# Optimization experiments

Measured on AMD Instinct MI355X. Metric: run time of the kernel, lower is better.

The kernel has to match this reference:

```python
import jax, jax.numpy as jnp
import numpy as np

N_NODES = 50000
N_EDGES = 800000
D_NODE = 128
D_EDGE = 128
D_OUT = 256
HID = 256


def setup_inputs() -> dict:
    key = jax.random.key(0)
    ks = jax.random.split(key, 10)
    s1 = 1.0 / np.sqrt(D_NODE + D_EDGE)
    s2 = 1.0 / np.sqrt(HID)
    s3 = 1.0 / np.sqrt(D_NODE + HID)
    return {
        "x": jax.random.normal(ks[0], (N_NODES, D_NODE), dtype=jnp.float32),
        "edge_index": jax.random.randint(ks[1], (2, N_EDGES), 0, N_NODES, dtype=jnp.int64),
        "edge_attr": jax.random.normal(ks[2], (N_EDGES, D_EDGE), dtype=jnp.float32),
        "u": jax.random.normal(ks[3], (1, 64), dtype=jnp.float32),
        "batch": jnp.zeros((N_NODES,), dtype=jnp.int64),
        "w1a": jax.random.normal(ks[4], (D_NODE + D_EDGE, HID), dtype=jnp.float32) * s1,
        "b1a": jnp.zeros((HID,), dtype=jnp.float32),
        "w1b": jax.random.normal(ks[5], (HID, HID), dtype=jnp.float32) * s2,
        "b1b": jnp.zeros((HID,), dtype=jnp.float32),
        "w2a": jax.random.normal(ks[6], (D_NODE + HID, HID), dtype=jnp.float32) * s3,
        "b2a": jnp.zeros((HID,), dtype=jnp.float32),
        "w2b": jax.random.normal(ks[7], (HID, D_OUT), dtype=jnp.float32) * s2,
        "b2b": jnp.zeros((D_OUT,), dtype=jnp.float32),
    }


def reference(x, edge_index, edge_attr, u, batch, w1a, b1a, w1b, b1b, w2a, b2a, w2b, b2b):
    row, col = edge_index[0], edge_index[1]
    # edge-wise MLP: [E, D_NODE + D_EDGE] -> 256 -> 256
    h = jnp.concatenate([x[row], edge_attr], axis=1)
    h = jax.nn.elu(h @ w1a + b1a) @ w1b + b1b  # [E, 256]
    # scatter_mean over destination nodes (dim_size = N)
    n = x.shape[0]
    sums = jax.ops.segment_sum(h, col, num_segments=n)  # [N, 256]
    cnt = jax.ops.segment_sum(jnp.ones((h.shape[0],), h.dtype), col, num_segments=n)
    mean = sums / jnp.maximum(cnt, 1.0)[:, None]
    # node-wise MLP: [N, D_NODE + 256] -> 256 -> D_OUT
    z = jnp.concatenate([x, mean], axis=1)
    return jax.nn.elu(z @ w2a + b2a) @ w2b + b2b
```

## Files before the change

### kernel.cpp

```cpp
#include <hip/hip_runtime.h>
#include <hip/hip_bf16.h>

#define N_NODES 50000
#define N_EDGES 800000

typedef short s16x8 __attribute__((ext_vector_type(8)));
typedef short s16x4 __attribute__((ext_vector_type(4)));
typedef float f32x4 __attribute__((ext_vector_type(4)));

__device__ __forceinline__ unsigned short f2bf(float f) {
    union { float f; unsigned u; } v; v.f = f;
    unsigned r = v.u + 0x7fffu + ((v.u >> 16) & 1u);
    return (unsigned short)(r >> 16);
}

__device__ __forceinline__ float bf2f(unsigned short u) {
    union { unsigned u; float f; } v; v.u = ((unsigned)u) << 16;
    return v.f;
}

__device__ __forceinline__ s16x8 ld8(const unsigned short* p) {
    return *(const s16x8*)p;
}

__device__ __forceinline__ float elu(float h) {
    return h > 0.0f ? h : (__expf(h) - 1.0f);
}

__global__ void wconv_kernel(const float* __restrict__ src,
                             unsigned short* __restrict__ dst,
                             int K, int N) {
    int idx = blockIdx.x * 256 + threadIdx.x;
    if (idx >= K * N) return;
    int n = idx / K;
    int k = idx - n * K;
    dst[idx] = f2bf(src[k * N + n]);
}

__global__ void hist_kernel(const int* __restrict__ ei, int* __restrict__ hist) {
    int e = blockIdx.x * 256 + threadIdx.x;
    if (e < N_EDGES) atomicAdd(&hist[ei[N_EDGES + e]], 1);
}

__global__ void scan_kernel(const int* __restrict__ hist, int* __restrict__ cursor) {
    __shared__ int tmp[1024];
    __shared__ int carryS;
    const int t = threadIdx.x;
    if (t == 0) carryS = 0;
    __syncthreads();
    for (int base = 0; base < N_NODES; base += 4096) {
        int i = base + t * 4;
        int4 v = {0, 0, 0, 0};
        if (i + 3 < N_NODES) v = *(const int4*)&hist[i];
        else {
            v.x = (i + 0 < N_NODES) ? hist[i + 0] : 0;
            v.y = (i + 1 < N_NODES) ? hist[i + 1] : 0;
            v.z = (i + 2 < N_NODES) ? hist[i + 2] : 0;
            v.w = (i + 3 < N_NODES) ? hist[i + 3] : 0;
        }
        int s = v.x + v.y + v.z + v.w;
        tmp[t] = s;
        __syncthreads();
        for (int off = 1; off < 1024; off <<= 1) {
            int add = (t >= off) ? tmp[t - off] : 0;
            __syncthreads();
            tmp[t] += add;
            __syncthreads();
        }
        int incl = tmp[t];
        int excl0 = carryS + incl - s;
        if (i     < N_NODES) cursor[i]     = excl0;
        if (i + 1 < N_NODES) cursor[i + 1] = excl0 + v.x;
        if (i + 2 < N_NODES) cursor[i + 2] = excl0 + v.x + v.y;
        if (i + 3 < N_NODES) cursor[i + 3] = excl0 + v.x + v.y + v.z;
        __syncthreads();
        if (t == 1023) carryS += incl;
        __syncthreads();
    }
}

__global__ void scatter_kernel(const int* __restrict__ ei, int* __restrict__ cursor,
                               int* __restrict__ sidx) {
    int e = blockIdx.x * 256 + threadIdx.x;
    if (e >= N_EDGES) return;
    int c = ei[N_EDGES + e];
    int p = atomicAdd(&cursor[c], 1);
    sidx[p] = e;
}

#define EP 264

__global__ __launch_bounds__(256, 4) void edge_kernel(
    const float* __restrict__ x, const int* __restrict__ ei,
    const float* __restrict__ ea, const int* __restrict__ sidx,
    const float* __restrict__ b1a,
    const unsigned short* __restrict__ w1aT,
    float* __restrict__ sums)
{
    __shared__ unsigned short lA[64 * EP];
    __shared__ int lrow[64];
    __shared__ int lcol[64];
    __shared__ int lidx[64];
    __shared__ unsigned char segstart[64];
    const int t = threadIdx.x;
    const int e0 = blockIdx.x * 64;

    if (t < 64) {
        int idx = sidx[e0 + t];
        lidx[t] = idx;
        lrow[t] = ei[idx];
        lcol[t] = ei[N_EDGES + idx];
    }
    __syncthreads();
    if (t < 64) segstart[t] = (t == 0) ? 1 : (lcol[t] != lcol[t - 1]);

    const f32x4* x4 = (const f32x4*)x;
    const f32x4* ea4 = (const f32x4*)ea;
#pragma unroll
    for (int i = 0; i < 8; i++) {
        int idx = i * 256 + t, r = idx >> 5, c4 = idx & 31;
        f32x4 v = x4[lrow[r] * 32 + c4];
        s16x4 b = { (short)f2bf(v.x), (short)f2bf(v.y), (short)f2bf(v.z), (short)f2bf(v.w) };
        *(s16x4*)&lA[r * EP + c4 * 4] = b;
    }
#pragma unroll
    for (int i = 0; i < 8; i++) {
        int idx = i * 256 + t, r = idx >> 5, c4 = idx & 31;
        f32x4 v = ea4[lidx[r] * 32 + c4];
        s16x4 b = { (short)f2bf(v.x), (short)f2bf(v.y), (short)f2bf(v.z), (short)f2bf(v.w) };
        *(s16x4*)&lA[r * EP + 128 + c4 * 4] = b;
    }
    __syncthreads();

    const int wv = t >> 6, lane = t & 63;
    const int quad = lane >> 4, l15 = lane & 15;

    f32x4 acc[4][4];
#pragma unroll
    for (int m = 0; m < 4; m++)
#pragma unroll
        for (int n = 0; n < 4; n++)
            acc[m][n] = (f32x4){0.f, 0.f, 0.f, 0.f};

    for (int kk = 0; kk < 8; kk++) {
        s16x8 a[4], b[4];
#pragma unroll
        for (int m = 0; m < 4; m++)
            a[m] = *(const s16x8*)&lA[(m * 16 + l15) * EP + kk * 32 + quad * 8];
#pragma unroll
        for (int n = 0; n < 4; n++)
            b[n] = ld8(&w1aT[(wv * 64 + n * 16 + l15) * 256 + kk * 32 + quad * 8]);
#pragma unroll
        for (int m = 0; m < 4; m++)
#pragma unroll
            for (int n = 0; n < 4; n++)
                acc[m][n] = __builtin_amdgcn_mfma_f32_16x16x32_bf16(a[m], b[n], acc[m][n], 0, 0, 0);
    }

    __syncthreads();

#pragma unroll
    for (int m = 0; m < 4; m++)
#pragma unroll
        for (int n = 0; n < 4; n++) {
            int col = wv * 64 + n * 16 + l15;
            float bias = b1a[col];
#pragma unroll
            for (int v = 0; v < 4; v++) {
                int row = m * 16 + quad * 4 + v;
                float h = elu(acc[m][n][v] + bias);
                lA[row * EP + col] = f2bf(h);
            }
        }
    __syncthreads();

    float s = 0.f;
    for (int r = 0; r < 64; r++) {
        if (r > 0 && segstart[r]) {
            atomicAdd(&sums[lcol[r - 1] * 256 + t], s);
            s = 0.f;
        }
        s += bf2f(lA[r * EP + t]);
    }
    atomicAdd(&sums[lcol[63] * 256 + t], s);
}

#define NP 392

__global__ __launch_bounds__(256, 3) void node_kernel(
    const float* __restrict__ x, const float* __restrict__ sums,
    const int* __restrict__ hist,
    const float* __restrict__ b1b, const float* __restrict__ b2a,
    const float* __restrict__ b2b,
    const unsigned short* __restrict__ w1bT, const unsigned short* __restrict__ w2aT,
    const unsigned short* __restrict__ w2bT,
    float* __restrict__ out)
{
    __shared__ unsigned short lZ[64 * NP];
    __shared__ float linv[64];
    __shared__ unsigned char lpos[64];
    const int t = threadIdx.x;
    const int n0 = blockIdx.x * 64;

    if (t < 64) {
        int c = 0;
        if (n0 + t < N_NODES) c = hist[n0 + t];
        lpos[t] = (c > 0);
        linv[t] = 1.0f / fmaxf((float)c, 1.0f);
    }
    __syncthreads();

#pragma unroll
    for (int i = 0; i < 8; i++) {
        int idx = i * 256 + t, r = idx >> 5, c4 = idx & 31;
        int node = n0 + r;
        f32x4 v = {0.f, 0.f, 0.f, 0.f};
        if (node < N_NODES) v = ((const f32x4*)x)[node * 32 + c4];
        s16x4 b = { (short)f2bf(v.x), (short)f2bf(v.y), (short)f2bf(v.z), (short)f2bf(v.w) };
        *(s16x4*)&lZ[r * NP + c4 * 4] = b;
    }
#pragma unroll
    for (int i = 0; i < 16; i++) {
        int idx = i * 256 + t, r = idx >> 6, c4 = idx & 63;
        int node = n0 + r;
        f32x4 v = {0.f, 0.f, 0.f, 0.f};
        if (node < N_NODES) v = ((const f32x4*)sums)[node * 64 + c4];
        float sc = linv[r];
        s16x4 b = { (short)f2bf(v.x * sc), (short)f2bf(v.y * sc),
                    (short)f2bf(v.z * sc), (short)f2bf(v.w * sc) };
        *(s16x4*)&lZ[r * NP + 128 + c4 * 4] = b;
    }
    __syncthreads();

    const int wv = t >> 6, lane = t & 63;
    const int quad = lane >> 4, l15 = lane & 15;

    f32x4 acc[4][4];
#pragma unroll
    for (int m = 0; m < 4; m++)
#pragma unroll
        for (int n = 0; n < 4; n++)
            acc[m][n] = (f32x4){0.f, 0.f, 0.f, 0.f};

    for (int kk = 0; kk < 8; kk++) {
        s16x8 a[4], b[4];
#pragma unroll
        for (int m = 0; m < 4; m++)
            a[m] = *(const s16x8*)&lZ[(m * 16 + l15) * NP + 128 + kk * 32 + quad * 8];
#pragma unroll
        for (int n = 0; n < 4; n++)
            b[n] = ld8(&w1bT[(wv * 64 + n * 16 + l15) * 256 + kk * 32 + quad * 8]);
#pragma unroll
        for (int m = 0; m < 4; m++)
#pragma unroll
            for (int n = 0; n < 4; n++)
                acc[m][n] = __builtin_amdgcn_mfma_f32_16x16x32_bf16(a[m], b[n], acc[m][n], 0, 0, 0);
    }
    __syncthreads();

#pragma unroll
    for (int m = 0; m < 4; m++)
#pragma unroll
        for (int n = 0; n < 4; n++) {
            int col = wv * 64 + n * 16 + l15;
            float bias = b1b[col];
#pragma unroll
            for (int v = 0; v < 4; v++) {
                int row = m * 16 + quad * 4 + v;
                float h = acc[m][n][v] + (lpos[row] ? bias : 0.f);
                lZ[row * NP + 128 + col] = f2bf(h);
            }
            acc[m][n] = (f32x4){0.f, 0.f, 0.f, 0.f};
        }
    __syncthreads();

    for (int kk = 0; kk < 12; kk++) {
        s16x8 a[4], b[4];
#pragma unroll
        for (int m = 0; m < 4; m++)
            a[m] = *(const s16x8*)&lZ[(m * 16 + l15) * NP + kk * 32 + quad * 8];
#pragma unroll
        for (int n = 0; n < 4; n++)
            b[n] = ld8(&w2aT[(wv * 64 + n * 16 + l15) * 384 + kk * 32 + quad * 8]);
#pragma unroll
        for (int m = 0; m < 4; m++)
#pragma unroll
            for (int n = 0; n < 4; n++)
                acc[m][n] = __builtin_amdgcn_mfma_f32_16x16x32_bf16(a[m], b[n], acc[m][n], 0, 0, 0);
    }
    __syncthreads();

#pragma unroll
    for (int m = 0; m < 4; m++)
#pragma unroll
        for (int n = 0; n < 4; n++) {
            int col = wv * 64 + n * 16 + l15;
            float bias = b2a[col];
#pragma unroll
            for (int v = 0; v < 4; v++) {
                int row = m * 16 + quad * 4 + v;
                float h = elu(acc[m][n][v] + bias);
                lZ[row * NP + col] = f2bf(h);
            }
            acc[m][n] = (f32x4){0.f, 0.f, 0.f, 0.f};
        }
    __syncthreads();

    for (int kk = 0; kk < 8; kk++) {
        s16x8 a[4], b[4];
#pragma unroll
        for (int m = 0; m < 4; m++)
            a[m] = *(const s16x8*)&lZ[(m * 16 + l15) * NP + kk * 32 + quad * 8];
#pragma unroll
        for (int n = 0; n < 4; n++)
            b[n] = ld8(&w2bT[(wv * 64 + n * 16 + l15) * 256 + kk * 32 + quad * 8]);
#pragma unroll
        for (int m = 0; m < 4; m++)
#pragma unroll
            for (int n = 0; n < 4; n++)
                acc[m][n] = __builtin_amdgcn_mfma_f32_16x16x32_bf16(a[m], b[n], acc[m][n], 0, 0, 0);
    }

#pragma unroll
    for (int m = 0; m < 4; m++)
#pragma unroll
        for (int n = 0; n < 4; n++) {
            int col = wv * 64 + n * 16 + l15;
            float bias = b2b[col];
#pragma unroll
            for (int v = 0; v < 4; v++) {
                int row = m * 16 + quad * 4 + v;
                int node = n0 + row;
                if (node < N_NODES)
                    out[node * 256 + col] = acc[m][n][v] + bias;
            }
        }
}

#define WS_SUMS   0u
#define WS_HIST   51200000u
#define WS_ZERO_BYTES 51400000u
#define WS_CURSOR 51400000u
#define WS_SIDX   51600000u
#define WS_W1A    54800000u
#define WS_W1B    54931072u
#define WS_W2A    55062144u
#define WS_W2B    55258752u

extern "C" void kernel_launch(void* const* d_in, const int* in_sizes, int n_in,
                              void* d_out, int out_size, void* d_ws, size_t ws_size,
                              hipStream_t stream) {
    const float* x   = (const float*)d_in[0];
    const int*   ei  = (const int*)d_in[1];
    const float* ea  = (const float*)d_in[2];
    const float* w1a = (const float*)d_in[5];
    const float* b1a = (const float*)d_in[6];
    const float* w1b = (const float*)d_in[7];
    const float* b1b = (const float*)d_in[8];
    const float* w2a = (const float*)d_in[9];
    const float* b2a = (const float*)d_in[10];
    const float* w2b = (const float*)d_in[11];
    const float* b2b = (const float*)d_in[12];
    float* out = (float*)d_out;

    char* ws = (char*)d_ws;
    float* sums = (float*)(ws + WS_SUMS);
    int* hist   = (int*)(ws + WS_HIST);
    int* cursor = (int*)(ws + WS_CURSOR);
    int* sidx   = (int*)(ws + WS_SIDX);
    unsigned short* w1aT = (unsigned short*)(ws + WS_W1A);
    unsigned short* w1bT = (unsigned short*)(ws + WS_W1B);
    unsigned short* w2aT = (unsigned short*)(ws + WS_W2A);
    unsigned short* w2bT = (unsigned short*)(ws + WS_W2B);

    hipMemsetAsync(d_ws, 0, WS_ZERO_BYTES, stream);

    wconv_kernel<<<(256 * 256 + 255) / 256, 256, 0, stream>>>(w1a, w1aT, 256, 256);
    wconv_kernel<<<(256 * 256 + 255) / 256, 256, 0, stream>>>(w1b, w1bT, 256, 256);
    wconv_kernel<<<(384 * 256 + 255) / 256, 256, 0, stream>>>(w2a, w2aT, 384, 256);
    wconv_kernel<<<(256 * 256 + 255) / 256, 256, 0, stream>>>(w2b, w2bT, 256, 256);

    hist_kernel<<<(N_EDGES + 255) / 256, 256, 0, stream>>>(ei, hist);
    scan_kernel<<<1, 1024, 0, stream>>>(hist, cursor);
    scatter_kernel<<<(N_EDGES + 255) / 256, 256, 0, stream>>>(ei, cursor, sidx);

    edge_kernel<<<N_EDGES / 64, 256, 0, stream>>>(x, ei, ea, sidx, b1a, w1aT, sums);

    node_kernel<<<(N_NODES + 63) / 64, 256, 0, stream>>>(x, sums, hist, b1b, b2a, b2b,
                                                         w1bT, w2aT, w2bT, out);
}
```

Measured before the change: 976.5 us.

## Halve edge tile, precompute sorted row/col pairs, shuffle-based scan, transposed segment reduce

The scatter kernel now also writes each sorted edge's (row, col) pair. The edge kernel can then read them directly instead of doing a dependent gather through sidx into edge_index. The edge kernel processes 32 edges per block instead of 64, with a higher occupancy hint, and segment boundaries come from a wave ballot. The post-ELU tile is stored transposed in LDS so the segmented sum reads 4 values per vector load. The single-block scan is rewritten with wave shuffles instead of a 1024-wide LDS Hillis-Steele loop. The smaller tile doubles how often the w1a weights are reloaded per edge and adds more block-boundary atomics, in exchange for more resident blocks.

```diff
diff --git a/kernel.cpp b/kernel.cpp
--- a/kernel.cpp
+++ b/kernel.cpp
@@ -43,115 +43,132 @@
 }
 
 __global__ void scan_kernel(const int* __restrict__ hist, int* __restrict__ cursor) {
-    __shared__ int tmp[1024];
-    __shared__ int carryS;
-    const int t = threadIdx.x;
-    if (t == 0) carryS = 0;
+    __shared__ int wsum[16];
+    __shared__ int carry;
+    const int t = threadIdx.x, wv = t >> 6, lane = t & 63;
+    if (t == 0) carry = 0;
     __syncthreads();
     for (int base = 0; base < N_NODES; base += 4096) {
         int i = base + t * 4;
         int4 v = {0, 0, 0, 0};
         if (i + 3 < N_NODES) v = *(const int4*)&hist[i];
         else {
-            v.x = (i + 0 < N_NODES) ? hist[i + 0] : 0;
-            v.y = (i + 1 < N_NODES) ? hist[i + 1] : 0;
-            v.z = (i + 2 < N_NODES) ? hist[i + 2] : 0;
-            v.w = (i + 3 < N_NODES) ? hist[i + 3] : 0;
-        }
-        int s = v.x + v.y + v.z + v.w;
-        tmp[t] = s;
+            if (i + 0 < N_NODES) v.x = hist[i + 0];
+            if (i + 1 < N_NODES) v.y = hist[i + 1];
+            if (i + 2 < N_NODES) v.z = hist[i + 2];
+            if (i + 3 < N_NODES) v.w = hist[i + 3];
+        }
+        int tot = v.x + v.y + v.z + v.w;
+        int s = tot;
+#pragma unroll
+        for (int off = 1; off < 64; off <<= 1) {
+            int u = __shfl_up(s, off);
+            if (lane >= off) s += u;
+        }
+        if (lane == 63) wsum[wv] = s;
         __syncthreads();
-        for (int off = 1; off < 1024; off <<= 1) {
-            int add = (t >= off) ? tmp[t - off] : 0;
-            __syncthreads();
-            tmp[t] += add;
-            __syncthreads();
-        }
-        int incl = tmp[t];
-        int excl0 = carryS + incl - s;
-        if (i     < N_NODES) cursor[i]     = excl0;
-        if (i + 1 < N_NODES) cursor[i + 1] = excl0 + v.x;
-        if (i + 2 < N_NODES) cursor[i + 2] = excl0 + v.x + v.y;
-        if (i + 3 < N_NODES) cursor[i + 3] = excl0 + v.x + v.y + v.z;
+        if (t < 16) {
+            int w = wsum[t];
+#pragma unroll
+            for (int off = 1; off < 16; off <<= 1) {
+                int u = __shfl_up(w, off);
+                if (t >= off) w += u;
+            }
+            wsum[t] = w;
+        }
         __syncthreads();
-        if (t == 1023) carryS += incl;
+        int e0 = carry + (wv ? wsum[wv - 1] : 0) + (s - tot);
+        if (i + 0 < N_NODES) cursor[i + 0] = e0;
+        if (i + 1 < N_NODES) cursor[i + 1] = e0 + v.x;
+        if (i + 2 < N_NODES) cursor[i + 2] = e0 + v.x + v.y;
+        if (i + 3 < N_NODES) cursor[i + 3] = e0 + v.x + v.y + v.z;
         __syncthreads();
+        if (t == 0) carry += wsum[15];
+        __syncthreads();
     }
 }
 
 __global__ void scatter_kernel(const int* __restrict__ ei, int* __restrict__ cursor,
-                               int* __restrict__ sidx) {
+                               int* __restrict__ sidx, int2* __restrict__ rc) {
     int e = blockIdx.x * 256 + threadIdx.x;
     if (e >= N_EDGES) return;
+    int r = ei[e];
     int c = ei[N_EDGES + e];
     int p = atomicAdd(&cursor[c], 1);
     sidx[p] = e;
+    rc[p] = make_int2(r, c);
 }
 
 #define EP 264
-
-__global__ __launch_bounds__(256, 4) void edge_kernel(
-    const float* __restrict__ x, const int* __restrict__ ei,
-    const float* __restrict__ ea, const int* __restrict__ sidx,
+#define PH 36
+
+__global__ __launch_bounds__(256, 5) void edge_kernel(
+    const float* __restrict__ x,
+    const float* __restrict__ ea,
+    const int* __restrict__ sidx, const int2* __restrict__ rc,
     const float* __restrict__ b1a,
     const unsigned short* __restrict__ w1aT,
     float* __restrict__ sums)
 {
-    __shared__ unsigned short lA[64 * EP];
-    __shared__ int lrow[64];
-    __shared__ int lcol[64];
-    __shared__ int lidx[64];
-    __shared__ unsigned char segstart[64];
+    __shared__ unsigned short lS[256 * PH];
+    __shared__ int lrow[32];
+    __shared__ int lcol[32];
+    __shared__ int lidx[32];
     const int t = threadIdx.x;
-    const int e0 = blockIdx.x * 64;
-
-    if (t < 64) {
-        int idx = sidx[e0 + t];
-        lidx[t] = idx;
-        lrow[t] = ei[idx];
-        lcol[t] = ei[N_EDGES + idx];
-    }
-    __syncthreads();
-    if (t < 64) segstart[t] = (t == 0) ? 1 : (lcol[t] != lcol[t - 1]);
+    const int e0 = blockIdx.x * 32;
+
+    if (t < 32) {
+        int2 v = rc[e0 + t];
+        lrow[t] = v.x;
+        lcol[t] = v.y;
+        lidx[t] = sidx[e0 + t];
+    }
+    __syncthreads();
+
+    const int lane = t & 63;
+    bool pred = false;
+    if (lane < 32) pred = (lane == 0) || (lcol[lane] != lcol[lane - 1]);
+    unsigned long long bm = __ballot(pred);
+    unsigned mask = (unsigned)bm;
 
     const f32x4* x4 = (const f32x4*)x;
     const f32x4* ea4 = (const f32x4*)ea;
 #pragma unroll
-    for (int i = 0; i < 8; i++) {
+    for (int i = 0; i < 4; i++) {
         int idx = i * 256 + t, r = idx >> 5, c4 = idx & 31;
         f32x4 v = x4[lrow[r] * 32 + c4];
         s16x4 b = { (short)f2bf(v.x), (short)f2bf(v.y), (short)f2bf(v.z), (short)f2bf(v.w) };
-        *(s16x4*)&lA[r * EP + c4 * 4] = b;
-    }
-#pragma unroll
-    for (int i = 0; i < 8; i++) {
+        *(s16x4*)&lS[r * EP + c4 * 4] = b;
+    }
+#pragma unroll
+    for (int i = 0; i < 4; i++) {
         int idx = i * 256 + t, r = idx >> 5, c4 = idx & 31;
         f32x4 v = ea4[lidx[r] * 32 + c4];
         s16x4 b = { (short)f2bf(v.x), (short)f2bf(v.y), (short)f2bf(v.z), (short)f2bf(v.w) };
-        *(s16x4*)&lA[r * EP + 128 + c4 * 4] = b;
-    }
-    __syncthreads();
-
-    const int wv = t >> 6, lane = t & 63;
+        *(s16x4*)&lS[r * EP + 128 + c4 * 4] = b;
+    }
+    __syncthreads();
+
+    const int wv = t >> 6;
     const int quad = lane >> 4, l15 = lane & 15;
 
-    f32x4 acc[4][4];
-#pragma unroll
-    for (int m = 0; m < 4; m++)
+    f32x4 acc[2][4];
+#pragma unroll
+    for (int m = 0; m < 2; m++)
 #pragma unroll
         for (int n = 0; n < 4; n++)
             acc[m][n] = (f32x4){0.f, 0.f, 0.f, 0.f};
 
     for (int kk = 0; kk < 8; kk++) {
-        s16x8 a[4], b[4];
-#pragma unroll
-        for (int m = 0; m < 4; m++)
-            a[m] = *(const s16x8*)&lA[(m * 16 + l15) * EP + kk * 32 + quad * 8];
+        s16x8 a[2], b[4];
+#pragma unroll
+        for (int m = 0; m < 2; m++)
+            a[m] = *(const s16x8*)&lS[(m * 16 + l15) * EP + kk * 32 + quad * 8];
 #pragma unroll
         for (int n = 0; n < 4; n++)
             b[n] = ld8(&w1aT[(wv * 64 + n * 16 + l15) * 256 + kk * 32 + quad * 8]);
 #pragma unroll
-        for (int m = 0; m < 4; m++)
+        for (int m = 0; m < 2; m++)
 #pragma unroll
             for (int n = 0; n < 4; n++)
                 acc[m][n] = __builtin_amdgcn_mfma_f32_16x16x32_bf16(a[m], b[n], acc[m][n], 0, 0, 0);
@@ -160,7 +177,7 @@
     __syncthreads();
 
 #pragma unroll
-    for (int m = 0; m < 4; m++)
+    for (int m = 0; m < 2; m++)
 #pragma unroll
         for (int n = 0; n < 4; n++) {
             int col = wv * 64 + n * 16 + l15;
@@ -169,20 +186,26 @@
             for (int v = 0; v < 4; v++) {
                 int row = m * 16 + quad * 4 + v;
                 float h = elu(acc[m][n][v] + bias);
-                lA[row * EP + col] = f2bf(h);
+                lS[col * PH + row] = f2bf(h);
             }
         }
     __syncthreads();
 
     float s = 0.f;
-    for (int r = 0; r < 64; r++) {
-        if (r > 0 && segstart[r]) {
-            atomicAdd(&sums[lcol[r - 1] * 256 + t], s);
-            s = 0.f;
-        }
-        s += bf2f(lA[r * EP + t]);
-    }
-    atomicAdd(&sums[lcol[63] * 256 + t], s);
+#pragma unroll
+    for (int j = 0; j < 8; j++) {
+        s16x4 hv = *(const s16x4*)&lS[t * PH + j * 4];
+#pragma unroll
+        for (int v = 0; v < 4; v++) {
+            int r = j * 4 + v;
+            if (r > 0 && ((mask >> r) & 1)) {
+                atomicAdd(&sums[lcol[r - 1] * 256 + t], s);
+                s = 0.f;
+            }
+            s += bf2f((unsigned short)hv[v]);
+        }
+    }
+    atomicAdd(&sums[lcol[31] * 256 + t], s);
 }
 
 #define NP 392
@@ -342,10 +365,11 @@
 #define WS_ZERO_BYTES 51400000u
 #define WS_CURSOR 51400000u
 #define WS_SIDX   51600000u
-#define WS_W1A    54800000u
-#define WS_W1B    54931072u
-#define WS_W2A    55062144u
-#define WS_W2B    55258752u
+#define WS_RC     54800000u
+#define WS_W1A    61200000u
+#define WS_W1B    61331072u
+#define WS_W2A    61462144u
+#define WS_W2B    61658752u
 
 extern "C" void kernel_launch(void* const* d_in, const int* in_sizes, int n_in,
                               void* d_out, int out_size, void* d_ws, size_t ws_size,
@@ -368,6 +392,7 @@
     int* hist   = (int*)(ws + WS_HIST);
     int* cursor = (int*)(ws + WS_CURSOR);
     int* sidx   = (int*)(ws + WS_SIDX);
+    int2* rc    = (int2*)(ws + WS_RC);
     unsigned short* w1aT = (unsigned short*)(ws + WS_W1A);
     unsigned short* w1bT = (unsigned short*)(ws + WS_W1B);
     unsigned short* w2aT = (unsigned short*)(ws + WS_W2A);
@@ -382,9 +407,9 @@
 
     hist_kernel<<<(N_EDGES + 255) / 256, 256, 0, stream>>>(ei, hist);
     scan_kernel<<<1, 1024, 0, stream>>>(hist, cursor);
-    scatter_kernel<<<(N_EDGES + 255) / 256, 256, 0, stream>>>(ei, cursor, sidx);
-
-    edge_kernel<<<N_EDGES / 64, 256, 0, stream>>>(x, ei, ea, sidx, b1a, w1aT, sums);
+    scatter_kernel<<<(N_EDGES + 255) / 256, 256, 0, stream>>>(ei, cursor, sidx, rc);
+
+    edge_kernel<<<N_EDGES / 32, 256, 0, stream>>>(x, ea, sidx, rc, b1a, w1aT, sums);
 
     node_kernel<<<(N_NODES + 63) / 64, 256, 0, stream>>>(x, sums, hist, b1b, b2a, b2b,
                                                          w1bT, w2aT, w2bT, out);
```

After: 1.115 ms. 1.14x slower.
